# Performance work log

Measured on AMD Instinct MI355X. Metric: run time of the kernel, lower is better.

The kernel has to match this reference:

```python
import jax, jax.numpy as jnp
import numpy as np

B, R, C_M, C_Z, H, DH, NQP = 2, 384, 384, 128, 12, 32, 4
W_C = (2.0 / (9 * NQP)) ** (-0.5)   # (2/(9*n_qp))^-0.5
W_L = 3.0 ** 0.5                     # (1/3)^-0.5


def setup_inputs() -> dict:
    key = jax.random.key(0)
    ks = jax.random.split(key, 10)
    pair_rep = jax.random.normal(ks[0], (B, R, R, C_Z), jnp.float32)
    sing_rep = jax.random.normal(ks[1], (B, R, C_M), jnp.float32)
    m = jax.random.normal(ks[2], (B, R, 3, 3), jnp.float32)
    bbr, _ = jnp.linalg.qr(m)  # orthonormal backbone frames (B,R,3,3)
    bbt = jax.random.normal(ks[3], (B, R, 3), jnp.float32)
    s = 0.02
    W_qkv = jax.random.normal(ks[4], (C_M, DH * 3 * H), jnp.float32) * s
    W_qk = jax.random.normal(ks[5], (C_M, H * 2 * NQP * 3), jnp.float32) * s
    W_fc1 = jax.random.normal(ks[6], (C_Z, H), jnp.float32) * s
    b_fc1 = jnp.zeros((H,), jnp.float32)
    W0 = jax.random.normal(ks[7], (H * DH, C_M), jnp.float32) * s
    W1 = jax.random.normal(ks[8], (H * C_Z, C_M), jnp.float32) * s
    gamma = jax.random.uniform(ks[9], (1,), jnp.float32)
    return dict(pair_rep=pair_rep, sing_rep=sing_rep, bbr=bbr, bbt=bbt,
                W_qkv=W_qkv, W_qk=W_qk, W_fc1=W_fc1, b_fc1=b_fc1,
                W0=W0, W1=W1, gamma=gamma)


def reference(pair_rep, sing_rep, bbr, bbt, W_qkv, W_qk, W_fc1, b_fc1, W0, W1, gamma):
    # pair bias: fc1 then b i j h -> b h i j
    pair_bias = jnp.transpose(jnp.einsum('bijc,ch->bijh', pair_rep, W_fc1) + b_fc1,
                              (0, 3, 1, 2))                      # b h i j
    # scalar q/k/v: channel layout (dim_head, 3, heads)
    qkv = (sing_rep @ W_qkv).reshape(B, R, DH, 3, H)
    rq, rk, rv = (jnp.transpose(qkv[:, :, :, i, :], (0, 3, 1, 2)) for i in range(3))  # b h r d
    dot = jnp.einsum('bhid,bhjd->bhij', rq, rk) * DH ** (-0.5)
    # point q/k: channel layout (heads, 2, n_qp, 3)
    qk = (sing_rep @ W_qk).reshape(B, R, H, 2, NQP, 3)
    gq = jnp.transpose(qk[:, :, :, 0], (0, 3, 1, 2, 4))          # b p r h a
    gk = jnp.transpose(qk[:, :, :, 1], (0, 3, 1, 2, 4))
    # frame-transformed query/key points
    Tq = jnp.einsum('bprha,brak->phbrk', gq, bbr) + bbt          # p h b r 3
    Tk = jnp.einsum('bprha,brak->phbrk', gk, bbr) + bbt
    diff = Tq[:, :, :, :, None, :] - Tk[:, :, :, None, :, :]     # p h b i j 3
    sq = jnp.transpose(jnp.sum(diff * diff, axis=(0, -1)), (1, 0, 2, 3))  # b h i j
    head_w = jax.nn.softplus(gamma[0]) * W_C / 2                 # same scalar per head
    attn = jax.nn.softmax(W_L * (pair_bias + dot + head_w * sq), axis=-1)
    # pair-rep value aggregation -> W_1
    top = jnp.einsum('bhij,bijc->bihc', attn, pair_rep).reshape(B, R, H * C_Z) @ W1
    # scalar value aggregation -> W_0   (note: original adds these two only;
    # the point-value 'bot' branch is computed but unused in the output)
    out = jnp.transpose(jnp.einsum('bhij,bhjd->bhid', attn, rv),
                        (0, 2, 1, 3)).reshape(B, R, H * DH) @ W0
    return out + top
```

## Files before the change

kernel.cpp:

```cpp
#include <hip/hip_runtime.h>
#include <math.h>

#define Bb   2
#define Rr   384
#define CMd  384
#define CZ   128
#define Hh   12
#define DHd  32

#define WL           1.7320508075688772f
#define WC           4.242640687119285f
#define INV_SQRT_DH  0.17677669529663687f

#define SZ_R   (Bb*Hh*Rr*DHd)
#define SZ_T   (Bb*Hh*Rr*12)
#define SZ_S   (Bb*Hh*Rr)
#define SZ_A   ((long)Bb*Hh*Rr*Rr)
#define SZ_O   (Bb*Rr*Hh*DHd)

__global__ __launch_bounds__(64) void k_projgemm(
    const float* __restrict__ sing, const float* __restrict__ Wqkv,
    const float* __restrict__ Wqk, float* __restrict__ pbuf)
{
  const int t = threadIdx.x;
  const int m0 = blockIdx.x * 32;
  const int n0 = blockIdx.y * 32;
  const int ks = blockIdx.z;
  const int tx = t & 7, ty = t >> 3;
  __shared__ float As[32][36];
  __shared__ float Bs[32][36];
  float acc[4][4] = {};

  for (int kc = ks*192; kc < ks*192 + 192; kc += 32) {
    #pragma unroll
    for (int i = 0; i < 4; ++i) {
      int s = t + 64*i;
      int row = s >> 3, k4 = (s & 7) << 2;
      float4 v = *(const float4*)(sing + (long)(m0 + row)*384 + kc + k4);
      As[k4  ][row] = v.x; As[k4+1][row] = v.y;
      As[k4+2][row] = v.z; As[k4+3][row] = v.w;
    }
    #pragma unroll
    for (int i = 0; i < 4; ++i) {
      int s = t + 64*i;
      int k = s >> 3, c4 = (s & 7) << 2;
      const float* srcB = (n0 < 1152)
          ? Wqkv + (long)(kc + k)*1152 + n0 + c4
          : Wqk  + (long)(kc + k)*288 + (n0 - 1152) + c4;
      float4 w = *(const float4*)srcB;
      Bs[k][c4] = w.x; Bs[k][c4+1] = w.y; Bs[k][c4+2] = w.z; Bs[k][c4+3] = w.w;
    }
    __syncthreads();
    #pragma unroll
    for (int k = 0; k < 32; ++k) {
      float4 a = *(const float4*)&As[k][ty*4];
      float4 b = *(const float4*)&Bs[k][tx*4];
      acc[0][0] += a.x*b.x; acc[0][1] += a.x*b.y; acc[0][2] += a.x*b.z; acc[0][3] += a.x*b.w;
      acc[1][0] += a.y*b.x; acc[1][1] += a.y*b.y; acc[1][2] += a.y*b.z; acc[1][3] += a.y*b.w;
      acc[2][0] += a.z*b.x; acc[2][1] += a.z*b.y; acc[2][2] += a.z*b.z; acc[2][3] += a.z*b.w;
      acc[3][0] += a.w*b.x; acc[3][1] += a.w*b.y; acc[3][2] += a.w*b.z; acc[3][3] += a.w*b.w;
    }
    __syncthreads();
  }
  float* pd = pbuf + (long)ks * (768*1440);
  #pragma unroll
  for (int i = 0; i < 4; ++i)
    *(float4*)&pd[(long)(m0 + ty*4 + i)*1440 + n0 + tx*4] =
        make_float4(acc[i][0], acc[i][1], acc[i][2], acc[i][3]);
}

__global__ __launch_bounds__(256) void k_scatter(
    const float* __restrict__ pbuf,
    float* __restrict__ rq, float* __restrict__ rk, float* __restrict__ rv,
    float* __restrict__ gbuf)
{
  const int idx = blockIdx.x*256 + threadIdx.x;
  const int row = idx / 360;
  const int n   = (idx - row*360) * 4;
  float4 a = ((const float4*)pbuf)[idx];
  float4 b = ((const float4*)(pbuf + (long)768*1440))[idx];
  float v[4] = {a.x + b.x, a.y + b.y, a.z + b.z, a.w + b.w};
  const int bb = row / Rr, rr = row - bb*Rr;
  #pragma unroll
  for (int j = 0; j < 4; ++j) {
    int nj = n + j;
    if (nj < 1152) {
      int d = nj/36, rem = nj - d*36, wh = rem/12, h = rem - wh*12;
      float* dst = (wh == 0) ? rq : (wh == 1) ? rk : rv;
      dst[(((long)bb*Hh + h)*Rr + rr)*DHd + d] = v[j];
    } else {
      gbuf[(long)row*288 + nj - 1152] = v[j];
    }
  }
}

__global__ __launch_bounds__(256) void k_frame(
    const float* __restrict__ gbuf, const float* __restrict__ bbr,
    const float* __restrict__ bbt,
    float* __restrict__ TqF, float* __restrict__ TkF,
    float* __restrict__ Qsq, float* __restrict__ Ksq)
{
  const int idx = blockIdx.x*256 + threadIdx.x;
  const int row = idx / 24, q = idx - row*24;
  const int h = q >> 1, s2 = q & 1;
  const float* gp = gbuf + (long)row*288 + h*24 + s2*12;
  float rot[9], tr[3];
  #pragma unroll
  for (int a = 0; a < 9; ++a) rot[a] = bbr[(long)row*9 + a];
  #pragma unroll
  for (int a = 0; a < 3; ++a) tr[a] = bbt[(long)row*3 + a];
  const int b = row / Rr, r = row - b*Rr;
  float* T = s2 ? TkF : TqF;
  const long tb = (((long)b*Hh + h)*Rr + r)*12;
  float v[12]; float ss = 0.f;
  #pragma unroll
  for (int p = 0; p < 4; ++p)
    #pragma unroll
    for (int k2 = 0; k2 < 3; ++k2) {
      float x = gp[p*3+0]*rot[k2] + gp[p*3+1]*rot[3+k2] + gp[p*3+2]*rot[6+k2] + tr[k2];
      v[p*3+k2] = x; ss += x*x;
    }
  *(float4*)(T + tb)     = make_float4(v[0], v[1], v[2],  v[3]);
  *(float4*)(T + tb + 4) = make_float4(v[4], v[5], v[6],  v[7]);
  *(float4*)(T + tb + 8) = make_float4(v[8], v[9], v[10], v[11]);
  (s2 ? Ksq : Qsq)[((long)b*Hh + h)*Rr + r] = ss;
}

__global__ __launch_bounds__(256) void k_pbias(
    const float* __restrict__ pair, const float* __restrict__ Wfc1,
    const float* __restrict__ bfc1, float* __restrict__ pb)
{
  const int t = threadIdx.x;
  __shared__ __align__(16) float w_t[12*128];
  __shared__ float bias_l[12];
  for (int s = t; s < 1536; s += 256) {
    int h = s >> 7, c = s & 127;
    w_t[s] = Wfc1[c*12 + h];
  }
  if (t < 12) bias_l[t] = bfc1[t];
  __syncthreads();

  const long r0 = (long)blockIdx.x*256 + t;
  const float4* pr0 = (const float4*)pair + r0*32;
  float acc0[12] = {};
  #pragma unroll 4
  for (int cc = 0; cc < 32; ++cc) {
    float4 p0 = pr0[cc];
    #pragma unroll
    for (int h = 0; h < 12; ++h) {
      float4 wv = *(const float4*)&w_t[h*128 + cc*4];
      acc0[h] += p0.x*wv.x + p0.y*wv.y + p0.z*wv.z + p0.w*wv.w;
    }
  }
  int b0 = (int)(r0 / 147456); long rm = r0 - (long)b0*147456;
  int i0 = (int)(rm / 384), j0 = (int)(rm - i0*384);
  #pragma unroll
  for (int h = 0; h < 12; ++h)
    pb[(((long)b0*Hh + h)*Rr + i0)*Rr + j0] = acc0[h] + bias_l[h];
}

#define ITILE 8
__global__ __launch_bounds__(256) void k_scores(
    const float* __restrict__ rq, const float* __restrict__ rk,
    const float* __restrict__ TqF, const float* __restrict__ TkF,
    const float* __restrict__ Qsq, const float* __restrict__ Ksq,
    const float* __restrict__ gamma, float* __restrict__ attn)
{
  const int t = threadIdx.x;
  const int nt = Rr / ITILE;
  const int bh = blockIdx.x / nt;
  const int i0 = (blockIdx.x - bh*nt) * ITILE;
  __shared__ float rk_l[384][33];
  __shared__ float rq_l[32];
  __shared__ float tq_l[12];
  __shared__ float scal[1];
  __shared__ float redm[4], reds[4];

  for (int idx = t; idx < 384*32; idx += 256)
    rk_l[idx >> 5][idx & 31] = rk[(long)bh*Rr*DHd + idx];

  const float g0 = gamma[0];
  const float head_w = log1pf(__expf(g0)) * (WC * 0.5f);

  for (int ii = 0; ii < ITILE; ++ii) {
    const int i = i0 + ii;
    if (t < 32) rq_l[t] = rq[((long)bh*Rr + i)*DHd + t];
    if (t < 12) tq_l[t] = TqF[((long)bh*Rr + i)*12 + t];
    if (t == 0) scal[0] = Qsq[(long)bh*Rr + i];
    __syncthreads();
    const float qs = scal[0];
    const long rowbase = ((long)bh*Rr + i)*Rr;

    auto logit_at = [&](int j) -> float {
      float dt = 0.f;
      #pragma unroll
      for (int dd = 0; dd < 32; ++dd) dt += rq_l[dd] * rk_l[j][dd];
      const float4* tk = (const float4*)(TkF + ((long)bh*Rr + j)*12);
      float4 ta = tk[0], tb = tk[1], tc = tk[2];
      float pt = tq_l[0]*ta.x + tq_l[1]*ta.y + tq_l[2]*ta.z + tq_l[3]*ta.w
               + tq_l[4]*tb.x + tq_l[5]*tb.y + tq_l[6]*tb.z + tq_l[7]*tb.w
               + tq_l[8]*tc.x + tq_l[9]*tc.y + tq_l[10]*tc.z + tq_l[11]*tc.w;
      float sqv = qs + Ksq[(long)bh*Rr + j] - 2.f*pt;
      return WL * (attn[rowbase + j] + dt*INV_SQRT_DH + head_w*sqv);
    };

    float l0 = logit_at(t);
    float l1 = (t < 128) ? logit_at(t + 256) : -3.4e38f;
    float m = fmaxf(l0, l1);
    #pragma unroll
    for (int s = 32; s; s >>= 1) m = fmaxf(m, __shfl_xor(m, s, 64));
    if ((t & 63) == 0) redm[t >> 6] = m;
    __syncthreads();
    m = fmaxf(fmaxf(redm[0], redm[1]), fmaxf(redm[2], redm[3]));
    float e0 = __expf(l0 - m);
    float e1 = (t < 128) ? __expf(l1 - m) : 0.f;
    float s = e0 + e1;
    #pragma unroll
    for (int sh = 32; sh; sh >>= 1) s += __shfl_xor(s, sh, 64);
    if ((t & 63) == 0) reds[t >> 6] = s;
    __syncthreads();
    float inv = 1.f / (reds[0] + reds[1] + reds[2] + reds[3]);
    attn[rowbase + t] = e0 * inv;
    if (t < 128) attn[rowbase + t + 256] = e1 * inv;
    __syncthreads();
  }
}

__global__ __launch_bounds__(256) void k_agg(
    const float* __restrict__ attn, const float* __restrict__ pair,
    const float* __restrict__ rv, float* __restrict__ o_ihd, float* __restrict__ top)
{
  const int t = threadIdx.x;
  const int bi = blockIdx.x;
  const int b = bi / Rr;
  const int i = bi - b*Rr;
  __shared__ float a_l[12][384];
  for (int idx = t; idx < 12*384; idx += 256) {
    int h = idx / 384, j = idx - h*384;
    a_l[h][j] = attn[(((long)b*Hh + h)*Rr + i)*Rr + j];
  }
  __syncthreads();
  const int c = t & 127, hh = t >> 7;
  const float* prow = pair + (long)bi * Rr * CZ;
  float acc0=0,acc1=0,acc2=0,acc3=0,acc4=0,acc5=0;
  for (int j = 0; j < 384; ++j) {
    float v = prow[(long)j*CZ + c];
    acc0 += a_l[hh   ][j]*v;
    acc1 += a_l[hh+2 ][j]*v;
    acc2 += a_l[hh+4 ][j]*v;
    acc3 += a_l[hh+6 ][j]*v;
    acc4 += a_l[hh+8 ][j]*v;
    acc5 += a_l[hh+10][j]*v;
  }
  float* tp = top + ((long)bi*Hh)*CZ + c;
  tp[(long)(hh   )*CZ] = acc0;
  tp[(long)(hh+2 )*CZ] = acc1;
  tp[(long)(hh+4 )*CZ] = acc2;
  tp[(long)(hh+6 )*CZ] = acc3;
  tp[(long)(hh+8 )*CZ] = acc4;
  tp[(long)(hh+10)*CZ] = acc5;
  for (int o = t; o < 384; o += 256) {
    int h = o >> 5, dd = o & 31;
    const float* rvp = rv + ((long)b*Hh + h)*Rr*DHd + dd;
    float s = 0.f;
    for (int j = 0; j < 384; ++j) s += a_l[h][j] * rvp[(long)j*DHd];
    o_ihd[(long)bi*384 + o] = s;
  }
}

#define K5_KSPLIT 6
#define K5_KLEN   320
__global__ __launch_bounds__(64) void k_final_part(
    const float* __restrict__ o_ihd, const float* __restrict__ top,
    const float* __restrict__ W0, const float* __restrict__ W1,
    float* __restrict__ partial)
{
  const int t = threadIdx.x;
  const int m0 = blockIdx.x * 32;
  const int n0 = blockIdx.y * 32;
  const int ks = blockIdx.z;
  const int tx = t & 7, ty = t >> 3;
  __shared__ float As[32][36];
  __shared__ float Bs[32][36];
  float acc[4][4] = {};

  for (int kc = ks*K5_KLEN; kc < ks*K5_KLEN + K5_KLEN; kc += 32) {
    #pragma unroll
    for (int i = 0; i < 4; ++i) {
      int s = t + 64*i;
      int row = s >> 3, k4 = (s & 7) << 2;
      int gk = kc + k4;
      const float* srcA = (gk < 384)
          ? o_ihd + (long)(m0 + row)*384 + gk
          : top   + (long)(m0 + row)*1536 + (gk - 384);
      float4 v = *(const float4*)srcA;
      As[k4  ][row] = v.x; As[k4+1][row] = v.y;
      As[k4+2][row] = v.z; As[k4+3][row] = v.w;
    }
    #pragma unroll
    for (int i = 0; i < 4; ++i) {
      int s = t + 64*i;
      int k = s >> 3, c4 = (s & 7) << 2;
      int gk = kc + k;
      const float* srcB = (gk < 384)
          ? W0 + (long)gk*384 + n0 + c4
          : W1 + (long)(gk - 384)*384 + n0 + c4;
      float4 w = *(const float4*)srcB;
      Bs[k][c4] = w.x; Bs[k][c4+1] = w.y; Bs[k][c4+2] = w.z; Bs[k][c4+3] = w.w;
    }
    __syncthreads();
    #pragma unroll
    for (int k = 0; k < 32; ++k) {
      float4 a = *(const float4*)&As[k][ty*4];
      float4 b = *(const float4*)&Bs[k][tx*4];
      acc[0][0] += a.x*b.x; acc[0][1] += a.x*b.y; acc[0][2] += a.x*b.z; acc[0][3] += a.x*b.w;
      acc[1][0] += a.y*b.x; acc[1][1] += a.y*b.y; acc[1][2] += a.y*b.z; acc[1][3] += a.y*b.w;
      acc[2][0] += a.z*b.x; acc[2][1] += a.z*b.y; acc[2][2] += a.z*b.z; acc[2][3] += a.z*b.w;
      acc[3][0] += a.w*b.x; acc[3][1] += a.w*b.y; acc[3][2] += a.w*b.z; acc[3][3] += a.w*b.w;
    }
    __syncthreads();
  }
  float* pdst = partial + (long)ks * (768*384);
  #pragma unroll
  for (int i = 0; i < 4; ++i)
    *(float4*)&pdst[(long)(m0 + ty*4 + i)*384 + n0 + tx*4] =
        make_float4(acc[i][0], acc[i][1], acc[i][2], acc[i][3]);
}

__global__ __launch_bounds__(256) void k_final_reduce(
    const float* __restrict__ partial, float* __restrict__ out)
{
  const int idx = blockIdx.x*256 + threadIdx.x;
  float4 r = make_float4(0.f, 0.f, 0.f, 0.f);
  #pragma unroll
  for (int p = 0; p < K5_KSPLIT; ++p) {
    float4 a = ((const float4*)(partial + (long)p*768*384))[idx];
    r.x += a.x; r.y += a.y; r.z += a.z; r.w += a.w;
  }
  ((float4*)out)[idx] = r;
}

extern "C" void kernel_launch(void* const* d_in, const int* in_sizes, int n_in,
                              void* d_out, int out_size, void* d_ws, size_t ws_size,
                              hipStream_t stream)
{
  (void)in_sizes; (void)n_in; (void)out_size; (void)ws_size;
  const float* pair  = (const float*)d_in[0];
  const float* sing  = (const float*)d_in[1];
  const float* bbr   = (const float*)d_in[2];
  const float* bbt   = (const float*)d_in[3];
  const float* Wqkv  = (const float*)d_in[4];
  const float* Wqk   = (const float*)d_in[5];
  const float* Wfc1  = (const float*)d_in[6];
  const float* bfc1  = (const float*)d_in[7];
  const float* W0    = (const float*)d_in[8];
  const float* W1    = (const float*)d_in[9];
  const float* gamma = (const float*)d_in[10];
  float* out = (float*)d_out;

  float* ws    = (float*)d_ws;
  float* rq    = ws;
  float* rk    = rq  + SZ_R;
  float* rv    = rk  + SZ_R;
  float* TqF   = rv  + SZ_R;
  float* TkF   = TqF + SZ_T;
  float* Qsq   = TkF + SZ_T;
  float* Ksq   = Qsq + SZ_S;
  float* attn  = Ksq + SZ_S;
  float* o_ihd = attn + SZ_A;
  float* top   = o_ihd + SZ_O;
  float* gbuf  = o_ihd;
  float* pbuf  = attn;
  float* partial = attn;

  k_projgemm<<<dim3(24, 45, 2), dim3(64), 0, stream>>>(sing, Wqkv, Wqk, pbuf);
  k_scatter<<<dim3(276480/256), dim3(256), 0, stream>>>(pbuf, rq, rk, rv, gbuf);
  k_frame<<<dim3(Bb*Rr*24/256), dim3(256), 0, stream>>>(
      gbuf, bbr, bbt, TqF, TkF, Qsq, Ksq);
  k_pbias<<<dim3(1152), dim3(256), 0, stream>>>(pair, Wfc1, bfc1, attn);
  k_scores<<<dim3(Bb*Hh*(Rr/ITILE)), dim3(256), 0, stream>>>(
      rq, rk, TqF, TkF, Qsq, Ksq, gamma, attn);
  k_agg<<<dim3(Bb*Rr), dim3(256), 0, stream>>>(attn, pair, rv, o_ihd, top);
  k_final_part<<<dim3(24, 12, K5_KSPLIT), dim3(64), 0, stream>>>(
      o_ihd, top, W0, W1, partial);
  k_final_reduce<<<dim3(768*384/4/256), dim3(256), 0, stream>>>(partial, out);
}
```

Measured before the change: 198.3 us.

## Coalesce pair-bias loads by splitting channels across 8 lanes with shuffle reduction

```diff
diff --git a/kernel.cpp b/kernel.cpp
--- a/kernel.cpp
+++ b/kernel.cpp
@@ -131,6 +131,7 @@
     const float* __restrict__ bfc1, float* __restrict__ pb)
 {
   const int t = threadIdx.x;
+  const int su = t & 7, rg = t >> 3;
   __shared__ __align__(16) float w_t[12*128];
   __shared__ float bias_l[12];
   for (int s = t; s < 1536; s += 256) {
@@ -140,23 +141,46 @@
   if (t < 12) bias_l[t] = bfc1[t];
   __syncthreads();
 
-  const long r0 = (long)blockIdx.x*256 + t;
-  const float4* pr0 = (const float4*)pair + r0*32;
-  float acc0[12] = {};
-  #pragma unroll 4
-  for (int cc = 0; cc < 32; ++cc) {
-    float4 p0 = pr0[cc];
+  const long rbase = (long)blockIdx.x * 128;
+  const float4* pr = (const float4*)pair;
+  float acc[4][12] = {};
+  #pragma unroll
+  for (int cc = 0; cc < 4; ++cc) {
+    const int f = su + 8*cc;
+    float4 p0 = pr[(rbase + rg      )*32 + f];
+    float4 p1 = pr[(rbase + rg + 32 )*32 + f];
+    float4 p2 = pr[(rbase + rg + 64 )*32 + f];
+    float4 p3 = pr[(rbase + rg + 96 )*32 + f];
     #pragma unroll
     for (int h = 0; h < 12; ++h) {
-      float4 wv = *(const float4*)&w_t[h*128 + cc*4];
-      acc0[h] += p0.x*wv.x + p0.y*wv.y + p0.z*wv.z + p0.w*wv.w;
-    }
-  }
-  int b0 = (int)(r0 / 147456); long rm = r0 - (long)b0*147456;
-  int i0 = (int)(rm / 384), j0 = (int)(rm - i0*384);
-  #pragma unroll
-  for (int h = 0; h < 12; ++h)
-    pb[(((long)b0*Hh + h)*Rr + i0)*Rr + j0] = acc0[h] + bias_l[h];
+      float4 wv = *(const float4*)&w_t[h*128 + f*4];
+      acc[0][h] += p0.x*wv.x + p0.y*wv.y + p0.z*wv.z + p0.w*wv.w;
+      acc[1][h] += p1.x*wv.x + p1.y*wv.y + p1.z*wv.z + p1.w*wv.w;
+      acc[2][h] += p2.x*wv.x + p2.y*wv.y + p2.z*wv.z + p2.w*wv.w;
+      acc[3][h] += p3.x*wv.x + p3.y*wv.y + p3.z*wv.z + p3.w*wv.w;
+    }
+  }
+  #pragma unroll
+  for (int rr = 0; rr < 4; ++rr)
+    #pragma unroll
+    for (int h = 0; h < 12; ++h) {
+      float v = acc[rr][h];
+      v += __shfl_xor(v, 1, 64);
+      v += __shfl_xor(v, 2, 64);
+      v += __shfl_xor(v, 4, 64);
+      acc[rr][h] = v;
+    }
+  if (su == 0) {
+    const int b0 = (int)(rbase / 147456);
+    const long ro = rbase - (long)b0*147456;
+    #pragma unroll
+    for (int rr = 0; rr < 4; ++rr) {
+      const long jrow = ro + rg + 32*rr;
+      #pragma unroll
+      for (int h = 0; h < 12; ++h)
+        pb[((long)b0*Hh + h)*147456 + jrow] = acc[rr][h] + bias_l[h];
+    }
+  }
 }
 
 #define ITILE 8
@@ -377,7 +401,7 @@
   k_scatter<<<dim3(276480/256), dim3(256), 0, stream>>>(pbuf, rq, rk, rv, gbuf);
   k_frame<<<dim3(Bb*Rr*24/256), dim3(256), 0, stream>>>(
       gbuf, bbr, bbt, TqF, TkF, Qsq, Ksq);
-  k_pbias<<<dim3(1152), dim3(256), 0, stream>>>(pair, Wfc1, bfc1, attn);
+  k_pbias<<<dim3(Bb*Rr*Rr/128), dim3(256), 0, stream>>>(pair, Wfc1, bfc1, attn);
   k_scores<<<dim3(Bb*Hh*(Rr/ITILE)), dim3(256), 0, stream>>>(
       rq, rk, TqF, TkF, Qsq, Ksq, gamma, attn);
   k_agg<<<dim3(Bb*Rr), dim3(256), 0, stream>>>(attn, pair, rv, o_ihd, top);
```

Measured after the change: 192.9 us. 1.03x faster.
